# Kernel tuning notes

Measured on AMD Instinct MI355X. Metric: run time of the kernel, lower is better.

## Reference

```python
import jax, jax.numpy as jnp
import numpy as np

DIM = 128
NH = 4
K = 7
PAD = K // 2  # dilation = 1
MLP_HID = 4 * DIM
EPS = 1e-5


def _layernorm(x, w, b):
    m = jnp.mean(x, axis=-1, keepdims=True)
    v = jnp.mean((x - m) ** 2, axis=-1, keepdims=True)
    return (x - m) / jnp.sqrt(v + EPS) * w + b


def _windows(xp, H, W):
    # xp: [B, nh, Hp, Wp, hd] zero-padded; returns [B, nh, H, W, hd, K*K]
    return jnp.stack(
        [xp[:, :, i:i + H, j:j + W, :] for i in range(K) for j in range(K)],
        axis=-1,
    )


def setup_inputs() -> dict:
    key = jax.random.key(0)
    ks = jax.random.split(key, 10)
    s = 0.02
    inp = {
        "x": jax.random.normal(ks[0], (4, 56, 56, DIM), dtype=jnp.float32),
        "ln1_w": jnp.ones((DIM,), jnp.float32),
        "ln1_b": jnp.zeros((DIM,), jnp.float32),
        "w_qkv": jax.random.normal(ks[1], (DIM, 3 * DIM), jnp.float32) * s,
        "b_qkv": jnp.zeros((3 * DIM,), jnp.float32),
        "rpb": jax.random.normal(ks[2], (NH, K * K), jnp.float32) * s,
        "w_proj": jax.random.normal(ks[3], (DIM, DIM), jnp.float32) * s,
        "b_proj": jnp.zeros((DIM,), jnp.float32),
        "ln2_w": jnp.ones((DIM,), jnp.float32),
        "ln2_b": jnp.zeros((DIM,), jnp.float32),
        "w_fc1": jax.random.normal(ks[4], (DIM, MLP_HID), jnp.float32) * s,
        "b_fc1": jnp.zeros((MLP_HID,), jnp.float32),
        "w_fc2": jax.random.normal(ks[5], (MLP_HID, DIM), jnp.float32) * s,
        "b_fc2": jnp.zeros((DIM,), jnp.float32),
    }
    return inp


def _nat_block(x, ln1_w, ln1_b, w_qkv, b_qkv, rpb, w_proj, b_proj,
               ln2_w, ln2_b, w_fc1, b_fc1, w_fc2, b_fc2):
    B, H, W, C = x.shape
    hd = C // NH
    scale = hd ** -0.5

    # --- neighborhood attention ---
    xn = _layernorm(x, ln1_w, ln1_b)
    qkv = xn @ w_qkv + b_qkv                       # [B,H,W,3C]
    qkv = qkv.reshape(B, H, W, 3, NH, hd)
    qkv = jnp.transpose(qkv, (3, 0, 4, 1, 2, 5))   # [3,B,nh,H,W,hd]
    q, k, v = qkv[0] * scale, qkv[1], qkv[2]
    # zero-pad spatial dims (matches F.pad with constant 0 in original)
    pad = ((0, 0), (0, 0), (PAD, PAD), (PAD, PAD), (0, 0))
    kp = jnp.pad(k, pad)
    vp = jnp.pad(v, pad)
    kw = _windows(kp, H, W)                        # [B,nh,H,W,hd,49]
    vw = _windows(vp, H, W)
    attn = jnp.einsum('bnhwd,bnhwdk->bnhwk', q, kw)
    attn = attn + rpb[None, :, None, None, :]
    attn = jax.nn.softmax(attn, axis=-1)
    out = jnp.einsum('bnhwk,bnhwdk->bnhwd', attn, vw)  # [B,nh,H,W,hd]
    out = jnp.transpose(out, (0, 2, 3, 1, 4)).reshape(B, H, W, C)
    x = x + (out @ w_proj + b_proj)

    # --- MLP ---
    xn2 = _layernorm(x, ln2_w, ln2_b)
    h = jax.nn.gelu(xn2 @ w_fc1 + b_fc1, approximate=False)
    x = x + (h @ w_fc2 + b_fc2)
    return x


def reference(x, ln1_w, ln1_b, w_qkv, b_qkv, rpb, w_proj, b_proj,
              ln2_w, ln2_b, w_fc1, b_fc1, w_fc2, b_fc2):
    return _nat_block(x, ln1_w, ln1_b, w_qkv, b_qkv, rpb, w_proj, b_proj,
                      ln2_w, ln2_b, w_fc1, b_fc1, w_fc2, b_fc2)
```

## Files before the change

kernel.cpp:

```cpp
#include <hip/hip_runtime.h>

#define TOKS 12544

using bf16x8 = __attribute__((ext_vector_type(8))) short;
using f32x4  = __attribute__((ext_vector_type(4))) float;
typedef unsigned short u16;
typedef __attribute__((ext_vector_type(8))) unsigned short u16x8;

__device__ __forceinline__ u16 f2b(float f){
  unsigned int i=__float_as_uint(f);
  return (u16)((i + 0x7FFFu + ((i>>16)&1u))>>16);
}
__device__ __forceinline__ float b2f(u16 u){
  union{unsigned int i; float f;}v; v.i=((unsigned int)u)<<16; return v.f;
}
__device__ __forceinline__ void async16(const void* g, void* l){
  __builtin_amdgcn_global_load_lds((__attribute__((address_space(1))) void*)(g),
                                   (__attribute__((address_space(3))) void*)(l), 16, 0, 0);
}

__global__ void prep_kernel(const float* __restrict__ wqkv, const float* __restrict__ wproj,
                            const float* __restrict__ wfc1, const float* __restrict__ wfc2,
                            u16* __restrict__ tqkv, u16* __restrict__ tproj,
                            u16* __restrict__ tfc1, u16* __restrict__ tfc2)
{
  int idx = blockIdx.x*256 + threadIdx.x;
  if (idx < 49152){ int n=idx>>7, k=idx&127; tqkv[idx]=f2b(wqkv[k*384+n]); }
  else if (idx < 65536){ int t=idx-49152; int n=t>>7, k=t&127; tproj[t]=f2b(wproj[k*128+n]); }
  else if (idx < 131072){ int t=idx-65536; int n=t>>7, k=t&127; tfc1[t]=f2b(wfc1[k*512+n]); }
  else if (idx < 196608){ int t=idx-131072; int n=t>>9, k=t&511; tfc2[t]=f2b(wfc2[k*128+n]); }
}

__global__ __launch_bounds__(256)
void ln_kernel(const float* __restrict__ xin, const float* __restrict__ w,
               const float* __restrict__ bia, u16* __restrict__ out)
{
  int lane = threadIdx.x & 63;
  int token = blockIdx.x*4 + (threadIdx.x>>6);
  float2 t = ((const float2*)xin)[token*64 + lane];
  float x0=t.x, x1=t.y;
  float s=x0+x1, q=x0*x0+x1*x1;
  #pragma unroll
  for (int off=32; off; off>>=1){ s+=__shfl_xor(s,off); q+=__shfl_xor(q,off); }
  float m = s*0.0078125f;
  float r = rsqrtf(q*0.0078125f - m*m + 1e-5f);
  int c = lane*2;
  ushort2 o;
  o.x = f2b((x0-m)*r*w[c]   + bia[c]);
  o.y = f2b((x1-m)*r*w[c+1] + bia[c+1]);
  ((ushort2*)out)[token*64+lane]=o;
}

#define M_QKV 0
#define M_PROJ 1
#define M_FC1 2
#define M_FC2 3

#define LNROW 148
#define LNGRP 36

template<int MODE>
__global__ __launch_bounds__(256)
void gemm_kernel(const u16* __restrict__ A, const u16* __restrict__ Bt,
                 const float* __restrict__ bias, int K,
                 const float* __restrict__ aux,
                 const float* __restrict__ lnw, const float* __restrict__ lnb,
                 float* __restrict__ fout,
                 u16* __restrict__ bout0,
                 u16* __restrict__ bout1, u16* __restrict__ bout2)
{
  constexpr int SMEM_BYTES = (MODE==M_PROJ) ? 64*LNROW*4 : 12288;
  __shared__ __align__(16) char smem[SMEM_BYTES];
  u16* lA = (u16*)smem;
  u16* lB = (u16*)(smem + 4096);

  const int tid=threadIdx.x;
  const int lane=tid&63, wid=tid>>6;
  const int quad=lane>>4, lrow=lane&15;
  const int m0=blockIdx.x*64, n0=blockIdx.y*128;
  const int wm=(wid&1)*32, wn=(wid>>1)*64;
  f32x4 acc[2][4] = {};

  const int rS=tid>>2, hS=tid&3;

  for (int k0=0;k0<K;k0+=32){
    async16(A  + (size_t)(m0+rS)*K    + k0 + hS*8, (char*)lA + tid*16);
    async16(Bt + (size_t)(n0+rS)*K    + k0 + hS*8, (char*)lB + tid*16);
    async16(Bt + (size_t)(n0+64+rS)*K + k0 + hS*8, (char*)lB + (tid+256)*16);
    __syncthreads();
    bf16x8 af[2], bfr[4];
    #pragma unroll
    for (int i=0;i<2;i++) af[i]  = ((const bf16x8*)lA)[(wm+i*16+lrow)*4 + quad];
    #pragma unroll
    for (int j=0;j<4;j++) bfr[j] = ((const bf16x8*)lB)[(wn+j*16+lrow)*4 + quad];
    #pragma unroll
    for (int i=0;i<2;i++)
      #pragma unroll
      for (int j=0;j<4;j++)
        acc[i][j] = __builtin_amdgcn_mfma_f32_16x16x32_bf16(af[i], bfr[j], acc[i][j], 0,0,0);
    __syncthreads();
  }

  const float scale = 0.17677669529663687f;
  float* sLN = (float*)smem;

  #pragma unroll
  for (int i=0;i<2;i++){
    #pragma unroll
    for (int j=0;j<4;j++){
      #pragma unroll
      for (int r=0;r<4;r++){
        int rl  = wm + i*16 + quad*4 + r;
        int row = m0 + rl;
        int col = n0 + wn + j*16 + lrow;
        float val = acc[i][j][r] + bias[col];
        if (MODE==M_QKV){
          int which = col>>7, ch = col&127;
          u16* dst = (which==0)? bout0 : ((which==1)? bout1 : bout2);
          if (which==0) val *= scale;
          dst[(size_t)row*128 + ch] = f2b(val);
        } else if (MODE==M_PROJ){
          val += aux[(size_t)row*128+col];
          sLN[rl*LNROW + (col>>5)*LNGRP + (col&31)] = val;
        } else if (MODE==M_FC1){
          float g = 0.5f*val*(1.0f+erff(val*0.70710678118654752f));
          bout0[(size_t)row*512+col]=f2b(g);
        } else {
          val += aux[(size_t)row*128+col];
          fout[(size_t)row*128+col]=val;
        }
      }
    }
  }

  if (MODE==M_PROJ){
    __syncthreads();
    int r2 = tid>>2, q = tid&3;
    const float* base = sLN + r2*LNROW + q*LNGRP;
    float v[32]; float s=0.f, sq=0.f;
    #pragma unroll
    for (int c4=0;c4<8;c4++){
      float4 t = ((const float4*)base)[c4];
      v[c4*4]=t.x; v[c4*4+1]=t.y; v[c4*4+2]=t.z; v[c4*4+3]=t.w;
      s += t.x+t.y+t.z+t.w;
      sq += t.x*t.x+t.y*t.y+t.z*t.z+t.w*t.w;
    }
    s  += __shfl_xor(s,1);  s  += __shfl_xor(s,2);
    sq += __shfl_xor(sq,1); sq += __shfl_xor(sq,2);
    float mean = s*0.0078125f;
    float rr = rsqrtf(sq*0.0078125f - mean*mean + 1e-5f);
    int row = m0 + r2;
    float* x1o = fout + (size_t)row*128 + q*32;
    u16*  xno = bout0 + (size_t)row*128 + q*32;
    #pragma unroll
    for (int c4=0;c4<8;c4++){
      float4 t; t.x=v[c4*4]; t.y=v[c4*4+1]; t.z=v[c4*4+2]; t.w=v[c4*4+3];
      ((float4*)x1o)[c4] = t;
      int col = q*32 + c4*4;
      ushort4 st;
      st.x = f2b((t.x-mean)*rr*lnw[col]   + lnb[col]);
      st.y = f2b((t.y-mean)*rr*lnw[col+1] + lnb[col+1]);
      st.z = f2b((t.z-mean)*rr*lnw[col+2] + lnb[col+2]);
      st.w = f2b((t.w-mean)*rr*lnw[col+3] + lnb[col+3]);
      ((ushort4*)xno)[c4] = st;
    }
  }
}

__global__ __launch_bounds__(256)
void attn_kernel(const u16* __restrict__ qb, const u16* __restrict__ kb,
                 const u16* __restrict__ vb, const float* __restrict__ rpb,
                 u16* __restrict__ aout)
{
  __shared__ __align__(16) u16 kt[196*32];
  __shared__ __align__(16) u16 vt[196*32];

  const int tid = threadIdx.x;
  const int tile = blockIdx.x;
  const int bh = blockIdx.y;
  const int b = bh>>2, h = bh&3;
  const int ty = (tile/7)*8, tx = (tile%7)*8;

  #pragma unroll
  for (int k=0;k<4;k++){
    int i = tid + k*256;
    if (i < 784){
      int pos = i>>2, c = i&3;
      int ly = pos/14, lx = pos-ly*14;
      int gy = ty + ly - 3, gx = tx + lx - 3;
      float4 kv = {0,0,0,0}, vv = {0,0,0,0};
      if (gy>=0 && gy<56 && gx>=0 && gx<56){
        size_t base = ((size_t)(b*3136 + gy*56 + gx)*128 + h*32 + c*8);
        kv = *(const float4*)(kb + base);
        vv = *(const float4*)(vb + base);
      }
      ((float4*)kt)[i] = kv;
      ((float4*)vt)[i] = vv;
    }
  }
  __syncthreads();

  const int px = tid>>2, q = tid&3;
  const int ly = px>>3, lx = px&7;
  const int tok = b*3136 + (ty+ly)*56 + (tx+lx);
  const int nbase = (ly*14 + lx)*32 + q*8;

  float qv[8];
  { u16x8 qq = *(const u16x8*)(qb + (size_t)tok*128 + h*32 + q*8);
    #pragma unroll
    for (int i=0;i<8;i++) qv[i]=b2f(qq[i]); }

  float sc[49];
  #pragma unroll
  for (int ky=0;ky<7;ky++){
    #pragma unroll
    for (int kx=0;kx<7;kx++){
      int n = ky*7+kx;
      u16x8 kk = *(const u16x8*)(kt + nbase + (ky*14+kx)*32);
      float s = 0.f;
      #pragma unroll
      for (int i=0;i<8;i++) s += qv[i]*b2f(kk[i]);
      s += __shfl_xor(s,1); s += __shfl_xor(s,2);
      sc[n] = s + rpb[h*49+n];
    }
  }
  float m=-1e30f;
  #pragma unroll
  for (int n=0;n<49;n++) m = fmaxf(m, sc[n]);
  float l=0.f;
  #pragma unroll
  for (int n=0;n<49;n++){ sc[n]=__expf(sc[n]-m); l+=sc[n]; }
  float inv = 1.f/l;

  float o[8]={};
  #pragma unroll
  for (int ky=0;ky<7;ky++){
    #pragma unroll
    for (int kx=0;kx<7;kx++){
      int n = ky*7+kx;
      u16x8 vv = *(const u16x8*)(vt + nbase + (ky*14+kx)*32);
      float p = sc[n];
      #pragma unroll
      for (int i=0;i<8;i++) o[i] += p*b2f(vv[i]);
    }
  }
  u16x8 ov;
  #pragma unroll
  for (int i=0;i<8;i++) ov[i] = f2b(o[i]*inv);
  *(u16x8*)(aout + (size_t)tok*128 + h*32 + q*8) = ov;
}

extern "C" void kernel_launch(void* const* d_in, const int* in_sizes, int n_in,
                              void* d_out, int out_size, void* d_ws, size_t ws_size,
                              hipStream_t stream)
{
  const float* x     =(const float*)d_in[0];
  const float* ln1w  =(const float*)d_in[1];
  const float* ln1b  =(const float*)d_in[2];
  const float* wqkv  =(const float*)d_in[3];
  const float* bqkv  =(const float*)d_in[4];
  const float* rpb   =(const float*)d_in[5];
  const float* wproj =(const float*)d_in[6];
  const float* bproj =(const float*)d_in[7];
  const float* ln2w  =(const float*)d_in[8];
  const float* ln2b  =(const float*)d_in[9];
  const float* wfc1  =(const float*)d_in[10];
  const float* bfc1  =(const float*)d_in[11];
  const float* wfc2  =(const float*)d_in[12];
  const float* bfc2  =(const float*)d_in[13];

  char* ws=(char*)d_ws;
  size_t o=0;
  u16* tqkv =(u16*)(ws+o); o+=98304;
  u16* tproj=(u16*)(ws+o); o+=32768;
  u16* tfc1 =(u16*)(ws+o); o+=131072;
  u16* tfc2 =(u16*)(ws+o); o+=131072;
  u16* xn   =(u16*)(ws+o); o+=3211264;
  u16* aout =(u16*)(ws+o); o+=3211264;
  u16* xn2  =(u16*)(ws+o); o+=3211264;
  u16* qb   =(u16*)(ws+o); o+=3211264;
  u16* kb   =(u16*)(ws+o); o+=3211264;
  u16* vb   =(u16*)(ws+o); o+=3211264;
  u16* hbuf =(u16*)(ws+o); o+=12845056;
  float* x1 =(float*)(ws+o); o+=6422528;

  prep_kernel<<<768,256,0,stream>>>(wqkv,wproj,wfc1,wfc2,tqkv,tproj,tfc1,tfc2);
  ln_kernel<<<3136,256,0,stream>>>(x,ln1w,ln1b,xn);
  gemm_kernel<M_QKV><<<dim3(196,3),256,0,stream>>>(xn,tqkv,bqkv,128,
      nullptr,nullptr,nullptr,nullptr, qb,kb,vb);
  attn_kernel<<<dim3(49,16),256,0,stream>>>(qb,kb,vb,rpb,aout);
  gemm_kernel<M_PROJ><<<dim3(196,1),256,0,stream>>>(aout,tproj,bproj,128,
      x, ln2w,ln2b, x1, xn2,nullptr,nullptr);
  gemm_kernel<M_FC1><<<dim3(196,4),256,0,stream>>>(xn2,tfc1,bfc1,128,
      nullptr,nullptr,nullptr,nullptr, hbuf,nullptr,nullptr);
  gemm_kernel<M_FC2><<<dim3(196,1),256,0,stream>>>(hbuf,tfc2,bfc2,512,
      x1,nullptr,nullptr, (float*)d_out, nullptr,nullptr,nullptr);
}
```

Measured before the change: 157.5 us.

## Fuse LN1 into QKV GEMM and fuse proj, LN2, FC1, FC2 into one kernel

```diff
diff --git a/kernel.cpp b/kernel.cpp
--- a/kernel.cpp
+++ b/kernel.cpp
@@ -1,6 +1,4 @@
 #include <hip/hip_runtime.h>
-
-#define TOKS 12544
 
 using bf16x8 = __attribute__((ext_vector_type(8))) short;
 using f32x4  = __attribute__((ext_vector_type(4))) float;
@@ -17,6 +15,13 @@
 __device__ __forceinline__ void async16(const void* g, void* l){
   __builtin_amdgcn_global_load_lds((__attribute__((address_space(1))) void*)(g),
                                    (__attribute__((address_space(3))) void*)(l), 16, 0, 0);
+}
+__device__ __forceinline__ float gelu_tanh(float v){
+  float u = v*(0.7978845608f + 0.0356774081f*v*v);
+  float e = __expf(-2.0f*fabsf(u));
+  float th = (1.0f-e)/(1.0f+e);
+  th = (u<0.f)? -th : th;
+  return 0.5f*v*(1.0f+th);
 }
 
 __global__ void prep_kernel(const float* __restrict__ wqkv, const float* __restrict__ wproj,
@@ -32,137 +37,98 @@
 }
 
 __global__ __launch_bounds__(256)
-void ln_kernel(const float* __restrict__ xin, const float* __restrict__ w,
-               const float* __restrict__ bia, u16* __restrict__ out)
+void qkv_ln_kernel(const float* __restrict__ x,
+                   const float* __restrict__ ln1w, const float* __restrict__ ln1b,
+                   const u16* __restrict__ tqkv, const float* __restrict__ bqkv,
+                   u16* __restrict__ qb, u16* __restrict__ kb, u16* __restrict__ vb)
 {
-  int lane = threadIdx.x & 63;
-  int token = blockIdx.x*4 + (threadIdx.x>>6);
-  float2 t = ((const float2*)xin)[token*64 + lane];
-  float x0=t.x, x1=t.y;
-  float s=x0+x1, q=x0*x0+x1*x1;
-  #pragma unroll
-  for (int off=32; off; off>>=1){ s+=__shfl_xor(s,off); q+=__shfl_xor(q,off); }
-  float m = s*0.0078125f;
-  float r = rsqrtf(q*0.0078125f - m*m + 1e-5f);
-  int c = lane*2;
-  ushort2 o;
-  o.x = f2b((x0-m)*r*w[c]   + bia[c]);
-  o.y = f2b((x1-m)*r*w[c+1] + bia[c+1]);
-  ((ushort2*)out)[token*64+lane]=o;
-}
-
-#define M_QKV 0
-#define M_PROJ 1
-#define M_FC1 2
-#define M_FC2 3
-
-#define LNROW 148
-#define LNGRP 36
-
-template<int MODE>
-__global__ __launch_bounds__(256)
-void gemm_kernel(const u16* __restrict__ A, const u16* __restrict__ Bt,
-                 const float* __restrict__ bias, int K,
-                 const float* __restrict__ aux,
-                 const float* __restrict__ lnw, const float* __restrict__ lnb,
-                 float* __restrict__ fout,
-                 u16* __restrict__ bout0,
-                 u16* __restrict__ bout1, u16* __restrict__ bout2)
-{
-  constexpr int SMEM_BYTES = (MODE==M_PROJ) ? 64*LNROW*4 : 12288;
-  __shared__ __align__(16) char smem[SMEM_BYTES];
-  u16* lA = (u16*)smem;
-  u16* lB = (u16*)(smem + 4096);
-
-  const int tid=threadIdx.x;
-  const int lane=tid&63, wid=tid>>6;
-  const int quad=lane>>4, lrow=lane&15;
-  const int m0=blockIdx.x*64, n0=blockIdx.y*128;
-  const int wm=(wid&1)*32, wn=(wid>>1)*64;
-  f32x4 acc[2][4] = {};
-
-  const int rS=tid>>2, hS=tid&3;
-
-  for (int k0=0;k0<K;k0+=32){
-    async16(A  + (size_t)(m0+rS)*K    + k0 + hS*8, (char*)lA + tid*16);
-    async16(Bt + (size_t)(n0+rS)*K    + k0 + hS*8, (char*)lB + tid*16);
-    async16(Bt + (size_t)(n0+64+rS)*K + k0 + hS*8, (char*)lB + (tid+256)*16);
-    __syncthreads();
-    bf16x8 af[2], bfr[4];
-    #pragma unroll
-    for (int i=0;i<2;i++) af[i]  = ((const bf16x8*)lA)[(wm+i*16+lrow)*4 + quad];
-    #pragma unroll
-    for (int j=0;j<4;j++) bfr[j] = ((const bf16x8*)lB)[(wn+j*16+lrow)*4 + quad];
-    #pragma unroll
-    for (int i=0;i<2;i++)
-      #pragma unroll
-      for (int j=0;j<4;j++)
-        acc[i][j] = __builtin_amdgcn_mfma_f32_16x16x32_bf16(af[i], bfr[j], acc[i][j], 0,0,0);
-    __syncthreads();
-  }
-
-  const float scale = 0.17677669529663687f;
-  float* sLN = (float*)smem;
-
-  #pragma unroll
-  for (int i=0;i<2;i++){
-    #pragma unroll
-    for (int j=0;j<4;j++){
-      #pragma unroll
-      for (int r=0;r<4;r++){
-        int rl  = wm + i*16 + quad*4 + r;
-        int row = m0 + rl;
-        int col = n0 + wn + j*16 + lrow;
-        float val = acc[i][j][r] + bias[col];
-        if (MODE==M_QKV){
-          int which = col>>7, ch = col&127;
-          u16* dst = (which==0)? bout0 : ((which==1)? bout1 : bout2);
-          if (which==0) val *= scale;
-          dst[(size_t)row*128 + ch] = f2b(val);
-        } else if (MODE==M_PROJ){
-          val += aux[(size_t)row*128+col];
-          sLN[rl*LNROW + (col>>5)*LNGRP + (col&31)] = val;
-        } else if (MODE==M_FC1){
-          float g = 0.5f*val*(1.0f+erff(val*0.70710678118654752f));
-          bout0[(size_t)row*512+col]=f2b(g);
-        } else {
-          val += aux[(size_t)row*128+col];
-          fout[(size_t)row*128+col]=val;
-        }
-      }
-    }
-  }
-
-  if (MODE==M_PROJ){
-    __syncthreads();
-    int r2 = tid>>2, q = tid&3;
-    const float* base = sLN + r2*LNROW + q*LNGRP;
-    float v[32]; float s=0.f, sq=0.f;
+  __shared__ __align__(16) char smem[49152];
+  char* lA = smem;
+  char* lB = smem + 16384;
+
+  const int tid = threadIdx.x;
+  const int lane = tid&63, wid = tid>>6;
+  const int quad = lane>>4, lrow = lane&15;
+  const int m0 = blockIdx.x*64;
+  const int wm = (wid&1)*32, wn = (wid>>1)*64;
+
+  {
+    const int row = tid>>2, q = tid&3;
+    float xv[32];
+    const float4* xr = (const float4*)(x + (size_t)(m0+row)*128 + q*32);
+    float s=0.f, sq=0.f;
     #pragma unroll
     for (int c4=0;c4<8;c4++){
-      float4 t = ((const float4*)base)[c4];
-      v[c4*4]=t.x; v[c4*4+1]=t.y; v[c4*4+2]=t.z; v[c4*4+3]=t.w;
+      float4 t = xr[c4];
+      xv[c4*4]=t.x; xv[c4*4+1]=t.y; xv[c4*4+2]=t.z; xv[c4*4+3]=t.w;
       s += t.x+t.y+t.z+t.w;
       sq += t.x*t.x+t.y*t.y+t.z*t.z+t.w*t.w;
     }
     s  += __shfl_xor(s,1);  s  += __shfl_xor(s,2);
     sq += __shfl_xor(sq,1); sq += __shfl_xor(sq,2);
     float mean = s*0.0078125f;
-    float rr = rsqrtf(sq*0.0078125f - mean*mean + 1e-5f);
-    int row = m0 + r2;
-    float* x1o = fout + (size_t)row*128 + q*32;
-    u16*  xno = bout0 + (size_t)row*128 + q*32;
+    float rstd = rsqrtf(sq*0.0078125f - mean*mean + 1e-5f);
+    const float4* wr = (const float4*)(ln1w + q*32);
+    const float4* br = (const float4*)(ln1b + q*32);
+    u16 nv[32];
     #pragma unroll
     for (int c4=0;c4<8;c4++){
-      float4 t; t.x=v[c4*4]; t.y=v[c4*4+1]; t.z=v[c4*4+2]; t.w=v[c4*4+3];
-      ((float4*)x1o)[c4] = t;
-      int col = q*32 + c4*4;
-      ushort4 st;
-      st.x = f2b((t.x-mean)*rr*lnw[col]   + lnb[col]);
-      st.y = f2b((t.y-mean)*rr*lnw[col+1] + lnb[col+1]);
-      st.z = f2b((t.z-mean)*rr*lnw[col+2] + lnb[col+2]);
-      st.w = f2b((t.w-mean)*rr*lnw[col+3] + lnb[col+3]);
-      ((ushort4*)xno)[c4] = st;
+      float4 w4 = wr[c4], b4 = br[c4];
+      nv[c4*4]   = f2b((xv[c4*4]  -mean)*rstd*w4.x + b4.x);
+      nv[c4*4+1] = f2b((xv[c4*4+1]-mean)*rstd*w4.y + b4.y);
+      nv[c4*4+2] = f2b((xv[c4*4+2]-mean)*rstd*w4.z + b4.z);
+      nv[c4*4+3] = f2b((xv[c4*4+3]-mean)*rstd*w4.w + b4.w);
+    }
+    #pragma unroll
+    for (int cc=0;cc<4;cc++){
+      u16x8 pk;
+      #pragma unroll
+      for (int e=0;e<8;e++) pk[e] = nv[cc*8+e];
+      *(u16x8*)(lA + (((q*4+cc)*64 + row)<<4)) = pk;
+    }
+  }
+
+  for (int nc=0; nc<3; nc++){
+    __syncthreads();
+    #pragma unroll
+    for (int kk=0;kk<8;kk++){
+      int i = tid + kk*256;
+      int n = i&127, c = i>>7;
+      async16(tqkv + (size_t)(nc*128+n)*128 + c*8, lB + i*16);
+    }
+    __syncthreads();
+
+    f32x4 acc[2][4] = {};
+    #pragma unroll
+    for (int ks=0;ks<4;ks++){
+      bf16x8 af[2], bfr[4];
+      #pragma unroll
+      for (int i=0;i<2;i++) af[i]  = ((const bf16x8*)lA)[(ks*4+quad)*64  + wm + i*16 + lrow];
+      #pragma unroll
+      for (int j=0;j<4;j++) bfr[j] = ((const bf16x8*)lB)[(ks*4+quad)*128 + wn + j*16 + lrow];
+      #pragma unroll
+      for (int i=0;i<2;i++)
+        #pragma unroll
+        for (int j=0;j<4;j++)
+          acc[i][j] = __builtin_amdgcn_mfma_f32_16x16x32_bf16(af[i], bfr[j], acc[i][j], 0,0,0);
+    }
+
+    const float scale = 0.17677669529663687f;
+    u16* dst = (nc==0)? qb : ((nc==1)? kb : vb);
+    #pragma unroll
+    for (int j=0;j<4;j++){
+      int col = wn + j*16 + lrow;
+      float bia = bqkv[nc*128 + col];
+      #pragma unroll
+      for (int i=0;i<2;i++){
+        #pragma unroll
+        for (int r=0;r<4;r++){
+          int row = m0 + wm + i*16 + quad*4 + r;
+          float val = acc[i][j][r] + bia;
+          if (nc==0) val *= scale;
+          dst[(size_t)row*128 + col] = f2b(val);
+        }
+      }
     }
   }
 }
@@ -248,6 +214,198 @@
   #pragma unroll
   for (int i=0;i<8;i++) ov[i] = f2b(o[i]*inv);
   *(u16x8*)(aout + (size_t)tok*128 + h*32 + q*8) = ov;
+}
+
+__global__ __launch_bounds__(256)
+void mega_mlp_kernel(const u16* __restrict__ aout, const float* __restrict__ x,
+                     const u16* __restrict__ tproj, const float* __restrict__ bproj,
+                     const float* __restrict__ ln2w, const float* __restrict__ ln2b,
+                     const u16* __restrict__ tfc1, const float* __restrict__ bfc1,
+                     const u16* __restrict__ tfc2, const float* __restrict__ bfc2,
+                     float* __restrict__ out)
+{
+  __shared__ __align__(16) char smem[65536];
+  char* lA  = smem;
+  char* lB  = smem + 16384;
+  char* xn2 = smem + 49152;
+
+  const int tid = threadIdx.x;
+  const int lane = tid&63, wid = tid>>6;
+  const int quad = lane>>4, lrow = lane&15;
+  const int m0 = blockIdx.x*64;
+  const int wm = (wid&1)*32, wn = (wid>>1)*64;
+  const int half = wid>>1;
+
+  #pragma unroll
+  for (int kk=0;kk<4;kk++){
+    int i = tid + kk*256;
+    int row = i&63, c = i>>6;
+    async16(aout + (size_t)(m0+row)*128 + c*8, lA + i*16);
+  }
+  #pragma unroll
+  for (int kk=0;kk<8;kk++){
+    int i = tid + kk*256;
+    int n = i&127, c = i>>7;
+    async16(tproj + (size_t)n*128 + c*8, lB + i*16);
+  }
+  __syncthreads();
+
+  f32x4 acc[2][4] = {};
+  #pragma unroll
+  for (int ks=0;ks<4;ks++){
+    bf16x8 af[2], bfr[4];
+    #pragma unroll
+    for (int i=0;i<2;i++) af[i]  = ((const bf16x8*)lA)[(ks*4+quad)*64  + wm + i*16 + lrow];
+    #pragma unroll
+    for (int j=0;j<4;j++) bfr[j] = ((const bf16x8*)lB)[(ks*4+quad)*128 + wn + j*16 + lrow];
+    #pragma unroll
+    for (int i=0;i<2;i++)
+      #pragma unroll
+      for (int j=0;j<4;j++)
+        acc[i][j] = __builtin_amdgcn_mfma_f32_16x16x32_bf16(af[i], bfr[j], acc[i][j], 0,0,0);
+  }
+  __syncthreads();
+
+  float x1v[2][4][4];
+  float ps[2][4] = {}, pq[2][4] = {};
+  #pragma unroll
+  for (int j=0;j<4;j++){
+    int col = wn + j*16 + lrow;
+    float bia = bproj[col];
+    #pragma unroll
+    for (int i=0;i<2;i++){
+      #pragma unroll
+      for (int r=0;r<4;r++){
+        int row = m0 + wm + i*16 + quad*4 + r;
+        float val = acc[i][j][r] + bia + x[(size_t)row*128 + col];
+        x1v[i][j][r] = val;
+        ps[i][r] += val; pq[i][r] += val*val;
+      }
+    }
+  }
+  #pragma unroll
+  for (int i=0;i<2;i++)
+    #pragma unroll
+    for (int r=0;r<4;r++){
+      #pragma unroll
+      for (int off=1; off<16; off<<=1){
+        ps[i][r] += __shfl_xor(ps[i][r], off);
+        pq[i][r] += __shfl_xor(pq[i][r], off);
+      }
+    }
+  float* redS = (float*)lA;
+  float* redQ = redS + 128;
+  if (lrow==0){
+    #pragma unroll
+    for (int i=0;i<2;i++)
+      #pragma unroll
+      for (int r=0;r<4;r++){
+        int row = wm + i*16 + quad*4 + r;
+        redS[half*64 + row] = ps[i][r];
+        redQ[half*64 + row] = pq[i][r];
+      }
+  }
+  __syncthreads();
+
+  {
+    float w2[4], b2[4];
+    #pragma unroll
+    for (int j=0;j<4;j++){ int col = wn+j*16+lrow; w2[j]=ln2w[col]; b2[j]=ln2b[col]; }
+    #pragma unroll
+    for (int i=0;i<2;i++){
+      #pragma unroll
+      for (int r=0;r<4;r++){
+        int row = wm + i*16 + quad*4 + r;
+        float mean = (redS[row] + redS[64+row])*0.0078125f;
+        float var  = (redQ[row] + redQ[64+row])*0.0078125f - mean*mean;
+        float rstd = rsqrtf(var + 1e-5f);
+        #pragma unroll
+        for (int j=0;j<4;j++){
+          int col = wn + j*16 + lrow;
+          u16 hv = f2b((x1v[i][j][r]-mean)*rstd*w2[j] + b2[j]);
+          ((u16*)xn2)[((col>>3)*64 + row)*8 + (col&7)] = hv;
+        }
+      }
+    }
+  }
+  __syncthreads();
+
+  f32x4 acc3[2][4] = {};
+  for (int nc=0; nc<4; nc++){
+    if (nc>0) __syncthreads();
+    #pragma unroll
+    for (int kk=0;kk<8;kk++){
+      int i = tid + kk*256;
+      int n = i&127, c = i>>7;
+      async16(tfc1 + (size_t)(nc*128+n)*128 + c*8, lB + i*16);
+    }
+    __syncthreads();
+
+    f32x4 acc2[2][4] = {};
+    #pragma unroll
+    for (int ks=0;ks<4;ks++){
+      bf16x8 af[2], bfr[4];
+      #pragma unroll
+      for (int i=0;i<2;i++) af[i]  = ((const bf16x8*)xn2)[(ks*4+quad)*64  + wm + i*16 + lrow];
+      #pragma unroll
+      for (int j=0;j<4;j++) bfr[j] = ((const bf16x8*)lB)[(ks*4+quad)*128 + wn + j*16 + lrow];
+      #pragma unroll
+      for (int i=0;i<2;i++)
+        #pragma unroll
+        for (int j=0;j<4;j++)
+          acc2[i][j] = __builtin_amdgcn_mfma_f32_16x16x32_bf16(af[i], bfr[j], acc2[i][j], 0,0,0);
+    }
+    #pragma unroll
+    for (int j=0;j<4;j++){
+      int col = wn + j*16 + lrow;
+      float bia = bfc1[nc*128 + col];
+      #pragma unroll
+      for (int i=0;i<2;i++){
+        #pragma unroll
+        for (int r=0;r<4;r++){
+          int row = wm + i*16 + quad*4 + r;
+          float g = gelu_tanh(acc2[i][j][r] + bia);
+          ((u16*)lA)[((col>>3)*64 + row)*8 + (col&7)] = f2b(g);
+        }
+      }
+    }
+    __syncthreads();
+    #pragma unroll
+    for (int kk=0;kk<8;kk++){
+      int i = tid + kk*256;
+      int n = i&127, c = i>>7;
+      async16(tfc2 + (size_t)n*512 + nc*128 + c*8, lB + i*16);
+    }
+    __syncthreads();
+
+    #pragma unroll
+    for (int ks=0;ks<4;ks++){
+      bf16x8 af[2], bfr[4];
+      #pragma unroll
+      for (int i=0;i<2;i++) af[i]  = ((const bf16x8*)lA)[(ks*4+quad)*64  + wm + i*16 + lrow];
+      #pragma unroll
+      for (int j=0;j<4;j++) bfr[j] = ((const bf16x8*)lB)[(ks*4+quad)*128 + wn + j*16 + lrow];
+      #pragma unroll
+      for (int i=0;i<2;i++)
+        #pragma unroll
+        for (int j=0;j<4;j++)
+          acc3[i][j] = __builtin_amdgcn_mfma_f32_16x16x32_bf16(af[i], bfr[j], acc3[i][j], 0,0,0);
+    }
+  }
+
+  #pragma unroll
+  for (int j=0;j<4;j++){
+    int col = wn + j*16 + lrow;
+    float bia = bfc2[col];
+    #pragma unroll
+    for (int i=0;i<2;i++){
+      #pragma unroll
+      for (int r=0;r<4;r++){
+        int row = m0 + wm + i*16 + quad*4 + r;
+        out[(size_t)row*128 + col] = acc3[i][j][r] + bia + x1v[i][j][r];
+      }
+    }
+  }
 }
 
 extern "C" void kernel_launch(void* const* d_in, const int* in_sizes, int n_in,
@@ -275,24 +433,14 @@
   u16* tproj=(u16*)(ws+o); o+=32768;
   u16* tfc1 =(u16*)(ws+o); o+=131072;
   u16* tfc2 =(u16*)(ws+o); o+=131072;
-  u16* xn   =(u16*)(ws+o); o+=3211264;
   u16* aout =(u16*)(ws+o); o+=3211264;
-  u16* xn2  =(u16*)(ws+o); o+=3211264;
   u16* qb   =(u16*)(ws+o); o+=3211264;
   u16* kb   =(u16*)(ws+o); o+=3211264;
   u16* vb   =(u16*)(ws+o); o+=3211264;
-  u16* hbuf =(u16*)(ws+o); o+=12845056;
-  float* x1 =(float*)(ws+o); o+=6422528;
 
   prep_kernel<<<768,256,0,stream>>>(wqkv,wproj,wfc1,wfc2,tqkv,tproj,tfc1,tfc2);
-  ln_kernel<<<3136,256,0,stream>>>(x,ln1w,ln1b,xn);
-  gemm_kernel<M_QKV><<<dim3(196,3),256,0,stream>>>(xn,tqkv,bqkv,128,
-      nullptr,nullptr,nullptr,nullptr, qb,kb,vb);
+  qkv_ln_kernel<<<196,256,0,stream>>>(x,ln1w,ln1b,tqkv,bqkv,qb,kb,vb);
   attn_kernel<<<dim3(49,16),256,0,stream>>>(qb,kb,vb,rpb,aout);
-  gemm_kernel<M_PROJ><<<dim3(196,1),256,0,stream>>>(aout,tproj,bproj,128,
-      x, ln2w,ln2b, x1, xn2,nullptr,nullptr);
-  gemm_kernel<M_FC1><<<dim3(196,4),256,0,stream>>>(xn2,tfc1,bfc1,128,
-      nullptr,nullptr,nullptr,nullptr, hbuf,nullptr,nullptr);
-  gemm_kernel<M_FC2><<<dim3(196,1),256,0,stream>>>(hbuf,tfc2,bfc2,512,
-      x1,nullptr,nullptr, (float*)d_out, nullptr,nullptr,nullptr);
-}
+  mega_mlp_kernel<<<196,256,0,stream>>>(aout,x,tproj,bproj,ln2w,ln2b,
+                                        tfc1,bfc1,tfc2,bfc2,(float*)d_out);
+}
```

Result: no change. 158.0 us (+0.3%).
